# Optimization experiments

Hardware: AMD Instinct MI355X
Metric: run time of the kernel (lower is better)

The kernel has to match this reference:

```python
import jax, jax.numpy as jnp
import numpy as np

N = 50000
E = 800000
D = 128
NEG_SLOPE = 0.2


def _gat_layer(x, W, al, ar, b, src, dst):
    """Single-head DGL-style GATConv with ReLU activation."""
    z = x @ W                                    # [N, D] projected features
    el = z @ al                                  # [N] left attention logits
    er = z @ ar                                  # [N] right attention logits
    e = jax.nn.leaky_relu(el[src] + er[dst], NEG_SLOPE)   # [E]
    # softmax over incoming edges per destination node (numerically stable)
    m = jax.ops.segment_max(e, dst, num_segments=N)       # [N]
    ex = jnp.exp(e - m[dst])                               # [E]
    s = jax.ops.segment_sum(ex, dst, num_segments=N)       # [N]
    alpha = ex / s[dst]                                    # [E]
    out = jax.ops.segment_sum(alpha[:, None] * z[src], dst, num_segments=N)  # [N, D]
    return jax.nn.relu(out + b)


def setup_inputs() -> dict:
    key = jax.random.key(0)
    ks = jax.random.split(key, 16)
    s = 0.05
    inp = {
        "f": jax.random.normal(ks[0], (N, D), dtype=jnp.float32),
        "src": jax.random.randint(ks[1], (E,), 0, N, dtype=jnp.int32),
        "dst": jax.random.randint(ks[2], (E,), 0, N, dtype=jnp.int32),
    }
    for i, kb in zip((1, 2, 3), (3, 7, 11)):
        inp[f"W{i}"] = jax.random.normal(ks[kb], (D, D), dtype=jnp.float32) * s
        inp[f"al{i}"] = jax.random.normal(ks[kb + 1], (D,), dtype=jnp.float32) * s
        inp[f"ar{i}"] = jax.random.normal(ks[kb + 2], (D,), dtype=jnp.float32) * s
        inp[f"b{i}"] = jnp.zeros((D,), dtype=jnp.float32)
    return inp


def reference(f, src, dst, W1, al1, ar1, b1, W2, al2, ar2, b2, W3, al3, ar3, b3):
    h = _gat_layer(f, W1, al1, ar1, b1, src, dst)
    h = _gat_layer(h, W2, al2, ar2, b2, src, dst)
    h = _gat_layer(h, W3, al3, ar3, b3, src, dst)
    return h  # [N, D] (single head already squeezed)
```

## Files before the change

### kernel.cpp

```cpp
#include <hip/hip_runtime.h>
#include <hip/hip_fp16.h>
#include <math.h>

#define NN 50000
#define NE 800000
#define DD 128
#define NEG_SLOPE 0.2f
#define CAP 64
#define GBLK ((NN + 63) / 64)
#define WSBLK (3 * 16384 / 256)
#define HBLK ((NE + 255) / 256)
#define SBLK ((NE + 511) / 512)
#define AGBLK ((NN + 31) / 32)

typedef short frag8 __attribute__((ext_vector_type(8)));
typedef float f32x4 __attribute__((ext_vector_type(4)));

__device__ __forceinline__ unsigned bf16_rne(float x) {
  unsigned u = __float_as_uint(x);
  return (u + 0x7FFFu + ((u >> 16) & 1u)) >> 16;
}

__device__ __forceinline__ void wsplit_body(
    int bid, const float* __restrict__ W0, const float* __restrict__ W1,
    const float* __restrict__ W2, short* __restrict__ Wh, short* __restrict__ Wl) {
  int gidx = bid * 256 + threadIdx.x;
  int L = gidx >> 14;
  int idx = gidx & 16383;
  const float* W = (L == 0) ? W0 : (L == 1) ? W1 : W2;
  int j = idx & 7;
  int lane = (idx >> 3) & 63;
  int tile = idx >> 9;
  int nt = tile & 7, kt = tile >> 3;
  int k = kt * 32 + (lane >> 4) * 8 + j;
  int n = nt * 16 + (lane & 15);
  float x = W[k * DD + n];
  unsigned hu = bf16_rne(x);
  float hf = __uint_as_float(hu << 16);
  unsigned lu = bf16_rne(x - hf);
  Wh[gidx] = (short)hu;
  Wl[gidx] = (short)lu;
}

__device__ __forceinline__ void hist_body(int bid, const int* __restrict__ dst,
                                          int* __restrict__ deg,
                                          unsigned short* __restrict__ edge_slot) {
  int i = bid * 256 + threadIdx.x;
  if (i < NE) edge_slot[i] = (unsigned short)atomicAdd(&deg[dst[i]], 1);
}

__global__ __launch_bounds__(256) void fused_pre(
    const float* __restrict__ W0, const float* __restrict__ W1, const float* __restrict__ W2,
    short* __restrict__ Wh, short* __restrict__ Wl,
    const int* __restrict__ dst, int* __restrict__ deg,
    unsigned short* __restrict__ edge_slot) {
  if (blockIdx.x < WSBLK) wsplit_body(blockIdx.x, W0, W1, W2, Wh, Wl);
  else hist_body(blockIdx.x - WSBLK, dst, deg, edge_slot);
}

__device__ __forceinline__ void gemm_body(
    int bid, short (*sB)[8192], float (*elp)[64], float (*erp)[64],
    const float* __restrict__ x, const short* __restrict__ Wh, const short* __restrict__ Wl,
    const float* __restrict__ al, const float* __restrict__ ar,
    __half* __restrict__ z, float* __restrict__ el, float* __restrict__ er) {
  const int t = threadIdx.x;
  const int w = t >> 6, lane = t & 63;
  const int m = lane & 15, quad = lane >> 4;
  const int half = w >> 2, mw = w & 3;
  const int ntb = half * 4;
  const int R0 = bid * 64 + mw * 16;

  auto stage = [&](int kt, int buf) {
    const uint4* gh = (const uint4*)(Wh + kt * 4096);
    const uint4* gl = (const uint4*)(Wl + kt * 4096);
    uint4* s = (uint4*)sB[buf];
    s[t] = gh[t];
    s[t + 512] = gl[t];
  };

  f32x4 acc[4];
#pragma unroll
  for (int n = 0; n < 4; n++) acc[n] = (f32x4)(0.f);

  int rA = R0 + m; if (rA > NN - 1) rA = NN - 1;

  stage(0, 0);
  __syncthreads();

#pragma unroll
  for (int kt = 0; kt < 4; kt++) {
    const int buf = kt & 1;
    if (kt < 3) stage(kt + 1, buf ^ 1);

    const float* xp = x + (size_t)rA * DD + kt * 32 + quad * 8;
    float xv[8];
    *(float4*)(xv) = *(const float4*)xp;
    *(float4*)(xv + 4) = *(const float4*)(xp + 4);
    frag8 ah, alo;
#pragma unroll
    for (int j = 0; j < 8; j++) {
      unsigned hu = bf16_rne(xv[j]);
      float hf = __uint_as_float(hu << 16);
      ah[j] = (short)hu;
      alo[j] = (short)bf16_rne(xv[j] - hf);
    }
#pragma unroll
    for (int n = 0; n < 4; n++) {
      frag8 bh = *(const frag8*)&sB[buf][(ntb + n) * 512 + lane * 8];
      frag8 bl = *(const frag8*)&sB[buf][4096 + (ntb + n) * 512 + lane * 8];
      acc[n] = __builtin_amdgcn_mfma_f32_16x16x32_bf16(alo, bh, acc[n], 0, 0, 0);
      acc[n] = __builtin_amdgcn_mfma_f32_16x16x32_bf16(ah, bl, acc[n], 0, 0, 0);
      acc[n] = __builtin_amdgcn_mfma_f32_16x16x32_bf16(ah, bh, acc[n], 0, 0, 0);
    }
    __syncthreads();
  }

  float alv[4], arv[4];
#pragma unroll
  for (int n = 0; n < 4; n++) {
    alv[n] = al[(ntb + n) * 16 + m];
    arv[n] = ar[(ntb + n) * 16 + m];
  }
#pragma unroll
  for (int r = 0; r < 4; r++) {
    float pl = 0.f, pr = 0.f;
#pragma unroll
    for (int n = 0; n < 4; n++) { pl += acc[n][r] * alv[n]; pr += acc[n][r] * arv[n]; }
#pragma unroll
    for (int off = 8; off; off >>= 1) {
      pl += __shfl_xor(pl, off, 64);
      pr += __shfl_xor(pr, off, 64);
    }
    int lrow = mw * 16 + quad * 4 + r;
    if (m == 0) { elp[half][lrow] = pl; erp[half][lrow] = pr; }
    int row = R0 + quad * 4 + r;
    if (row < NN) {
#pragma unroll
      for (int n = 0; n < 4; n++) {
        unsigned short hu = __half_as_ushort(__float2half(acc[n][r]));
        unsigned short hn = (unsigned short)__shfl_xor((int)hu, 1, 64);
        if ((m & 1) == 0) {
          __half2 pair = __halves2half2(__ushort_as_half(hu), __ushort_as_half(hn));
          *(__half2*)(z + (size_t)row * DD + (ntb + n) * 16 + m) = pair;
        }
      }
    }
  }
  __syncthreads();
  if (t < 64) {
    int row = bid * 64 + t;
    if (row < NN) {
      el[row] = elp[0][t] + elp[1][t];
      er[row] = erp[0][t] + erp[1][t];
    }
  }
}

__device__ __forceinline__ void scatter_body(
    int bid, const int* __restrict__ src, const int* __restrict__ dst,
    const unsigned short* __restrict__ edge_slot, unsigned short* __restrict__ csr_src) {
  int i = bid * 512 + threadIdx.x;
  if (i >= NE) return;
  int slot = edge_slot[i]; if (slot > CAP - 1) slot = CAP - 1;
  csr_src[dst[i] * CAP + slot] = (unsigned short)src[i];
}

__global__ __launch_bounds__(512) void fused_scatter_gemm(
    const float* __restrict__ x, const short* __restrict__ Wh, const short* __restrict__ Wl,
    const float* __restrict__ al, const float* __restrict__ ar,
    __half* __restrict__ z, float* __restrict__ el, float* __restrict__ er,
    const int* __restrict__ src, const int* __restrict__ dst,
    const unsigned short* __restrict__ edge_slot, unsigned short* __restrict__ csr_src) {
  __shared__ __align__(16) short sB[2][8192];
  __shared__ float elp[2][64], erp[2][64];
  if (blockIdx.x < GBLK) gemm_body(blockIdx.x, sB, elp, erp, x, Wh, Wl, al, ar, z, el, er);
  else scatter_body(blockIdx.x - GBLK, src, dst, edge_slot, csr_src);
}

__device__ __forceinline__ float2 agg_node(
    int node, int lane, const int* __restrict__ deg,
    const unsigned short* __restrict__ csr_src, const float* __restrict__ el,
    float erd, const __half* __restrict__ z, float* inv_s_out) {
  int dn = deg[node]; if (dn > CAP) dn = CAP;
  int beg = node * CAP;
  const __half2* zb = (const __half2*)z + lane;

  int sn = 0; float wv = 0.f;
  if (lane < dn) {
    sn = csr_src[beg + lane];
    float e = el[sn] + erd;
    e = (e > 0.f) ? e : NEG_SLOPE * e;
    wv = __expf(e);
  }
  float ssum = wv;

  float2 accA = make_float2(0.f, 0.f);
  float2 accB = make_float2(0.f, 0.f);
  for (int jj = 0; jj < dn; jj += 8) {
    float ww[8]; int ss[8];
#pragma unroll
    for (int u = 0; u < 8; u++) {
      ww[u] = __shfl(wv, jj + u, 64);
      ss[u] = __shfl(sn, jj + u, 64);
    }
    float2 zv[8];
#pragma unroll
    for (int u = 0; u < 8; u++) zv[u] = __half22float2(zb[(size_t)ss[u] * 64]);
#pragma unroll
    for (int u = 0; u < 8; u += 2) {
      accA.x += ww[u] * zv[u].x;     accA.y += ww[u] * zv[u].y;
      accB.x += ww[u + 1] * zv[u + 1].x; accB.y += ww[u + 1] * zv[u + 1].y;
    }
  }
  float2 acc = make_float2(accA.x + accB.x, accA.y + accB.y);
#pragma unroll
  for (int off = 32; off; off >>= 1) ssum += __shfl_xor(ssum, off, 64);
  *inv_s_out = (dn > 0) ? 1.f / ssum : 0.f;
  return acc;
}

__global__ __launch_bounds__(512) void agg_gemm(
    const int* __restrict__ deg, const unsigned short* __restrict__ csr_src,
    const float* __restrict__ el_in, const float* __restrict__ er_in,
    const __half* __restrict__ z_in, const float* __restrict__ bias,
    const short* __restrict__ Wh, const short* __restrict__ Wl,
    const float* __restrict__ al, const float* __restrict__ ar,
    __half* __restrict__ z_out, float* __restrict__ el_out, float* __restrict__ er_out) {
  __shared__ __align__(16) float hS[32][132];
  __shared__ float elp[4][32], erp[4][32];
  __shared__ int nq;

  const int t = threadIdx.x;
  const int w = t >> 6, lane = t & 63;
  const int R0 = blockIdx.x * 32;

  if (t == 0) nq = 0;
  float2 bv = *(const float2*)(bias + lane * 2);
  __syncthreads();

  for (;;) {
    int lrow;
    if (lane == 0) lrow = atomicAdd(&nq, 1);
    lrow = __builtin_amdgcn_readfirstlane(lrow);
    if (lrow >= 32) break;
    int node = R0 + lrow;
    float hx = 0.f, hy = 0.f;
    if (node < NN) {
      float inv_s;
      float2 acc = agg_node(node, lane, deg, csr_src, el_in, er_in[node], z_in, &inv_s);
      hx = fmaxf(acc.x * inv_s + bv.x, 0.f);
      hy = fmaxf(acc.y * inv_s + bv.y, 0.f);
    }
    *(float2*)&hS[lrow][lane * 2] = make_float2(hx, hy);
  }
  __syncthreads();

  const int m = lane & 15, quad = lane >> 4;
  const int mt = w >> 2, p = w & 3;
  const int nt0 = p, nt1 = p + 4;
  f32x4 acc0 = (f32x4)(0.f), acc1 = (f32x4)(0.f);

#pragma unroll
  for (int kt = 0; kt < 4; kt++) {
    const float* hp = &hS[mt * 16 + m][kt * 32 + quad * 8];
    float xv[8];
    *(float4*)(xv) = *(const float4*)hp;
    *(float4*)(xv + 4) = *(const float4*)(hp + 4);
    frag8 ah, alo;
#pragma unroll
    for (int j = 0; j < 8; j++) {
      unsigned hu = bf16_rne(xv[j]);
      float hf = __uint_as_float(hu << 16);
      ah[j] = (short)hu;
      alo[j] = (short)bf16_rne(xv[j] - hf);
    }
    const short* bhp = Wh + kt * 4096 + lane * 8;
    const short* blp = Wl + kt * 4096 + lane * 8;
    frag8 bh0 = *(const frag8*)(bhp + nt0 * 512);
    frag8 bl0 = *(const frag8*)(blp + nt0 * 512);
    frag8 bh1 = *(const frag8*)(bhp + nt1 * 512);
    frag8 bl1 = *(const frag8*)(blp + nt1 * 512);
    acc0 = __builtin_amdgcn_mfma_f32_16x16x32_bf16(alo, bh0, acc0, 0, 0, 0);
    acc0 = __builtin_amdgcn_mfma_f32_16x16x32_bf16(ah, bl0, acc0, 0, 0, 0);
    acc0 = __builtin_amdgcn_mfma_f32_16x16x32_bf16(ah, bh0, acc0, 0, 0, 0);
    acc1 = __builtin_amdgcn_mfma_f32_16x16x32_bf16(alo, bh1, acc1, 0, 0, 0);
    acc1 = __builtin_amdgcn_mfma_f32_16x16x32_bf16(ah, bl1, acc1, 0, 0, 0);
    acc1 = __builtin_amdgcn_mfma_f32_16x16x32_bf16(ah, bh1, acc1, 0, 0, 0);
  }

  float alv0 = al[nt0 * 16 + m], arv0 = ar[nt0 * 16 + m];
  float alv1 = al[nt1 * 16 + m], arv1 = ar[nt1 * 16 + m];
#pragma unroll
  for (int r = 0; r < 4; r++) {
    float pl = acc0[r] * alv0 + acc1[r] * alv1;
    float pr = acc0[r] * arv0 + acc1[r] * arv1;
#pragma unroll
    for (int off = 8; off; off >>= 1) {
      pl += __shfl_xor(pl, off, 64);
      pr += __shfl_xor(pr, off, 64);
    }
    int lrow = mt * 16 + quad * 4 + r;
    if (m == 0) { elp[p][lrow] = pl; erp[p][lrow] = pr; }
    int row = R0 + lrow;
    if (row < NN) {
      unsigned short hu0 = __half_as_ushort(__float2half(acc0[r]));
      unsigned short hn0 = (unsigned short)__shfl_xor((int)hu0, 1, 64);
      unsigned short hu1 = __half_as_ushort(__float2half(acc1[r]));
      unsigned short hn1 = (unsigned short)__shfl_xor((int)hu1, 1, 64);
      if ((m & 1) == 0) {
        *(__half2*)(z_out + (size_t)row * DD + nt0 * 16 + m) =
            __halves2half2(__ushort_as_half(hu0), __ushort_as_half(hn0));
        *(__half2*)(z_out + (size_t)row * DD + nt1 * 16 + m) =
            __halves2half2(__ushort_as_half(hu1), __ushort_as_half(hn1));
      }
    }
  }
  __syncthreads();
  if (t < 32) {
    int row = R0 + t;
    if (row < NN) {
      el_out[row] = elp[0][t] + elp[1][t] + elp[2][t] + elp[3][t];
      er_out[row] = erp[0][t] + erp[1][t] + erp[2][t] + erp[3][t];
    }
  }
}

__global__ __launch_bounds__(256) void gat_agg(
    const int* __restrict__ deg, const unsigned short* __restrict__ csr_src,
    const float* __restrict__ el, const float* __restrict__ er,
    const __half* __restrict__ z, const float* __restrict__ b,
    float* __restrict__ out) {
  int node = (int)((blockIdx.x * 256 + threadIdx.x) >> 6);
  int lane = threadIdx.x & 63;
  if (node >= NN) return;
  float inv_s;
  float2 acc = agg_node(node, lane, deg, csr_src, el, er[node], z, &inv_s);
  float2 bvv = *(const float2*)(b + lane * 2);
  float ox = fmaxf(acc.x * inv_s + bvv.x, 0.f);
  float oy = fmaxf(acc.y * inv_s + bvv.y, 0.f);
  *(float2*)(out + (size_t)node * DD + lane * 2) = make_float2(ox, oy);
}

extern "C" void kernel_launch(void* const* d_in, const int* in_sizes, int n_in,
                              void* d_out, int out_size, void* d_ws, size_t ws_size,
                              hipStream_t stream) {
  const float* f   = (const float*)d_in[0];
  const int*   src = (const int*)d_in[1];
  const int*   dst = (const int*)d_in[2];
  const float* W[3]  = {(const float*)d_in[3], (const float*)d_in[7],  (const float*)d_in[11]};
  const float* al[3] = {(const float*)d_in[4], (const float*)d_in[8],  (const float*)d_in[12]};
  const float* ar[3] = {(const float*)d_in[5], (const float*)d_in[9],  (const float*)d_in[13]};
  const float* bb[3] = {(const float*)d_in[6], (const float*)d_in[10], (const float*)d_in[14]};

  short* Wh3 = (short*)d_ws;
  short* Wl3 = Wh3 + 3 * 16384;
  __half* zA = (__half*)(Wl3 + 3 * 16384);
  __half* zB = zA + (size_t)NN * DD;
  float* el  = (float*)(zB + (size_t)NN * DD);
  float* er  = el + NN;
  float* el2 = er + NN;
  float* er2 = el2 + NN;
  int* deg = (int*)(er2 + NN);
  unsigned short* edge_slot = (unsigned short*)(deg + NN);
  unsigned short* csr_src   = edge_slot + NE;

  hipMemsetAsync(deg, 0, NN * sizeof(int), stream);
  fused_pre<<<WSBLK + HBLK, 256, 0, stream>>>(W[0], W[1], W[2], Wh3, Wl3, dst, deg, edge_slot);
  fused_scatter_gemm<<<GBLK + SBLK, 512, 0, stream>>>(f, Wh3, Wl3, al[0], ar[0],
                                                      zA, el, er,
                                                      src, dst, edge_slot, csr_src);
  agg_gemm<<<AGBLK, 512, 0, stream>>>(deg, csr_src, el, er, zA, bb[0],
                                      Wh3 + 16384, Wl3 + 16384, al[1], ar[1],
                                      zB, el2, er2);
  agg_gemm<<<AGBLK, 512, 0, stream>>>(deg, csr_src, el2, er2, zB, bb[1],
                                      Wh3 + 2 * 16384, Wl3 + 2 * 16384, al[2], ar[2],
                                      zA, el, er);
  gat_agg<<<(NN * 64) / 256, 256, 0, stream>>>(deg, csr_src, el, er, zA, bb[2],
                                               (float*)d_out);
}
```

Before: 281.5 us.

## Gather neighbor rows with 16-byte loads, four edges per wave in parallel

```diff
diff --git a/kernel.cpp b/kernel.cpp
--- a/kernel.cpp
+++ b/kernel.cpp
@@ -177,13 +177,14 @@
   else scatter_body(blockIdx.x - GBLK, src, dst, edge_slot, csr_src);
 }
 
-__device__ __forceinline__ float2 agg_node(
+__device__ __forceinline__ void agg_node16(
     int node, int lane, const int* __restrict__ deg,
     const unsigned short* __restrict__ csr_src, const float* __restrict__ el,
-    float erd, const __half* __restrict__ z, float* inv_s_out) {
+    float erd, const __half* __restrict__ z, float* out, float* inv_s_out) {
   int dn = deg[node]; if (dn > CAP) dn = CAP;
   int beg = node * CAP;
-  const __half2* zb = (const __half2*)z + lane;
+  const int g = lane >> 4, c16 = lane & 15;
+  const float4* zb = (const float4*)z;
 
   int sn = 0; float wv = 0.f;
   if (lane < dn) {
@@ -194,29 +195,39 @@
   }
   float ssum = wv;
 
-  float2 accA = make_float2(0.f, 0.f);
-  float2 accB = make_float2(0.f, 0.f);
+  float acc[8];
+#pragma unroll
+  for (int k = 0; k < 8; k++) acc[k] = 0.f;
+
   for (int jj = 0; jj < dn; jj += 8) {
-    float ww[8]; int ss[8];
-#pragma unroll
-    for (int u = 0; u < 8; u++) {
-      ww[u] = __shfl(wv, jj + u, 64);
-      ss[u] = __shfl(sn, jj + u, 64);
-    }
-    float2 zv[8];
-#pragma unroll
-    for (int u = 0; u < 8; u++) zv[u] = __half22float2(zb[(size_t)ss[u] * 64]);
-#pragma unroll
-    for (int u = 0; u < 8; u += 2) {
-      accA.x += ww[u] * zv[u].x;     accA.y += ww[u] * zv[u].y;
-      accB.x += ww[u + 1] * zv[u + 1].x; accB.y += ww[u + 1] * zv[u + 1].y;
-    }
-  }
-  float2 acc = make_float2(accA.x + accB.x, accA.y + accB.y);
+    float w0 = __shfl(wv, jj + g, 64);
+    int   s0 = __shfl(sn, jj + g, 64);
+    float w1 = __shfl(wv, jj + 4 + g, 64);
+    int   s1 = __shfl(sn, jj + 4 + g, 64);
+    float4 zv0 = zb[(size_t)s0 * 16 + c16];
+    float4 zv1 = zb[(size_t)s1 * 16 + c16];
+    const __half2* h0 = (const __half2*)&zv0;
+    const __half2* h1 = (const __half2*)&zv1;
+#pragma unroll
+    for (int k = 0; k < 4; k++) {
+      float2 f0 = __half22float2(h0[k]);
+      float2 f1 = __half22float2(h1[k]);
+      acc[2 * k]     += w0 * f0.x;
+      acc[2 * k + 1] += w0 * f0.y;
+      acc[2 * k]     += w1 * f1.x;
+      acc[2 * k + 1] += w1 * f1.y;
+    }
+  }
+#pragma unroll
+  for (int k = 0; k < 8; k++) {
+    acc[k] += __shfl_xor(acc[k], 16, 64);
+    acc[k] += __shfl_xor(acc[k], 32, 64);
+  }
 #pragma unroll
   for (int off = 32; off; off >>= 1) ssum += __shfl_xor(ssum, off, 64);
   *inv_s_out = (dn > 0) ? 1.f / ssum : 0.f;
-  return acc;
+#pragma unroll
+  for (int k = 0; k < 8; k++) out[k] = acc[k];
 }
 
 __global__ __launch_bounds__(512) void agg_gemm(
@@ -233,9 +244,11 @@
   const int t = threadIdx.x;
   const int w = t >> 6, lane = t & 63;
   const int R0 = blockIdx.x * 32;
+  const int c16 = lane & 15;
 
   if (t == 0) nq = 0;
-  float2 bv = *(const float2*)(bias + lane * 2);
+  float4 bv0 = ((const float4*)bias)[c16 * 2];
+  float4 bv1 = ((const float4*)bias)[c16 * 2 + 1];
   __syncthreads();
 
   for (;;) {
@@ -244,14 +257,23 @@
     lrow = __builtin_amdgcn_readfirstlane(lrow);
     if (lrow >= 32) break;
     int node = R0 + lrow;
-    float hx = 0.f, hy = 0.f;
+    float o[8] = {0.f, 0.f, 0.f, 0.f, 0.f, 0.f, 0.f, 0.f};
     if (node < NN) {
-      float inv_s;
-      float2 acc = agg_node(node, lane, deg, csr_src, el_in, er_in[node], z_in, &inv_s);
-      hx = fmaxf(acc.x * inv_s + bv.x, 0.f);
-      hy = fmaxf(acc.y * inv_s + bv.y, 0.f);
-    }
-    *(float2*)&hS[lrow][lane * 2] = make_float2(hx, hy);
+      float inv_s, a8[8];
+      agg_node16(node, lane, deg, csr_src, el_in, er_in[node], z_in, a8, &inv_s);
+      o[0] = fmaxf(a8[0] * inv_s + bv0.x, 0.f);
+      o[1] = fmaxf(a8[1] * inv_s + bv0.y, 0.f);
+      o[2] = fmaxf(a8[2] * inv_s + bv0.z, 0.f);
+      o[3] = fmaxf(a8[3] * inv_s + bv0.w, 0.f);
+      o[4] = fmaxf(a8[4] * inv_s + bv1.x, 0.f);
+      o[5] = fmaxf(a8[5] * inv_s + bv1.y, 0.f);
+      o[6] = fmaxf(a8[6] * inv_s + bv1.z, 0.f);
+      o[7] = fmaxf(a8[7] * inv_s + bv1.w, 0.f);
+    }
+    if (lane < 16) {
+      *(float4*)&hS[lrow][c16 * 8]     = make_float4(o[0], o[1], o[2], o[3]);
+      *(float4*)&hS[lrow][c16 * 8 + 4] = make_float4(o[4], o[5], o[6], o[7]);
+    }
   }
   __syncthreads();
 
@@ -333,12 +355,24 @@
   int node = (int)((blockIdx.x * 256 + threadIdx.x) >> 6);
   int lane = threadIdx.x & 63;
   if (node >= NN) return;
-  float inv_s;
-  float2 acc = agg_node(node, lane, deg, csr_src, el, er[node], z, &inv_s);
-  float2 bvv = *(const float2*)(b + lane * 2);
-  float ox = fmaxf(acc.x * inv_s + bvv.x, 0.f);
-  float oy = fmaxf(acc.y * inv_s + bvv.y, 0.f);
-  *(float2*)(out + (size_t)node * DD + lane * 2) = make_float2(ox, oy);
+  const int c16 = lane & 15;
+  float inv_s, a8[8];
+  agg_node16(node, lane, deg, csr_src, el, er[node], z, a8, &inv_s);
+  if (lane < 16) {
+    float4 bv0 = ((const float4*)b)[c16 * 2];
+    float4 bv1 = ((const float4*)b)[c16 * 2 + 1];
+    float4 o0, o1;
+    o0.x = fmaxf(a8[0] * inv_s + bv0.x, 0.f);
+    o0.y = fmaxf(a8[1] * inv_s + bv0.y, 0.f);
+    o0.z = fmaxf(a8[2] * inv_s + bv0.z, 0.f);
+    o0.w = fmaxf(a8[3] * inv_s + bv0.w, 0.f);
+    o1.x = fmaxf(a8[4] * inv_s + bv1.x, 0.f);
+    o1.y = fmaxf(a8[5] * inv_s + bv1.y, 0.f);
+    o1.z = fmaxf(a8[6] * inv_s + bv1.z, 0.f);
+    o1.w = fmaxf(a8[7] * inv_s + bv1.w, 0.f);
+    *(float4*)(out + (size_t)node * DD + c16 * 8)     = o0;
+    *(float4*)(out + (size_t)node * DD + c16 * 8 + 4) = o1;
+  }
 }
 
 extern "C" void kernel_launch(void* const* d_in, const int* in_sizes, int n_in,
```

Result: faster. 273.7 us (median of 2 runs) (-2.8%).
